# Kernel tuning notes

Hardware: AMD Instinct MI355X
Metric: run time of the kernel (lower is better)

Reference implementation:

```python
import jax, jax.numpy as jnp
import numpy as np

NUM_NODES = 1_000_000
MEM = 128
NODE_F = 172
EDGE_F = 172
EMB = 128
DECAY = 0.1
B = 16384


def setup_inputs() -> dict:
    key = jax.random.key(0)
    ks = jax.random.split(key, 32)
    g = lambda k, sh, s=0.05: (s * jax.random.normal(k, sh)).astype(jnp.float32)
    inp = {
        "src_ids": jax.random.randint(ks[0], (B,), 0, NUM_NODES),
        "dst_ids": jax.random.randint(ks[1], (B,), 0, NUM_NODES),
        "src_features": g(ks[2], (B, NODE_F), 1.0),
        "dst_features": g(ks[3], (B, NODE_F), 1.0),
        "timestamps": jax.random.uniform(ks[4], (B,), jnp.float32),
        "edge_features": g(ks[5], (B, EDGE_F), 1.0),
        # persistent state (pre-populated so decay math is non-trivial)
        "memory0": g(ks[6], (NUM_NODES, MEM), 1.0),
        "last_update0": jax.random.uniform(ks[7], (NUM_NODES,), jnp.float32),
        # edge_embedding
        "W_edge": g(ks[8], (EDGE_F, MEM)), "b_edge": jnp.zeros((MEM,), jnp.float32),
        # message_processor: Linear(MEM,MEM) -> relu -> Linear(MEM,MEM)
        "W_mp1": g(ks[9], (MEM, MEM)), "b_mp1": jnp.zeros((MEM,), jnp.float32),
        "W_mp2": g(ks[10], (MEM, MEM)), "b_mp2": jnp.zeros((MEM,), jnp.float32),
        # GRUCell(MEM, MEM), torch layout [3*MEM, MEM] (r,z,n)
        "W_ih": g(ks[11], (3 * MEM, MEM)), "W_hh": g(ks[12], (3 * MEM, MEM)),
        "b_ih": jnp.zeros((3 * MEM,), jnp.float32), "b_hh": jnp.zeros((3 * MEM,), jnp.float32),
        # node_embedding
        "W_node": g(ks[13], (NODE_F, MEM)), "b_node": jnp.zeros((MEM,), jnp.float32),
        # embedding_projection: Linear(2*MEM, EMB) -> relu -> Linear(EMB, EMB)
        "W_p1": g(ks[14], (2 * MEM, EMB)), "b_p1": jnp.zeros((EMB,), jnp.float32),
        "W_p2": g(ks[15], (EMB, EMB)), "b_p2": jnp.zeros((EMB,), jnp.float32),
        # link_predictor: Linear(2*EMB, EMB) -> relu -> Linear(EMB, 1) -> sigmoid
        "W_l1": g(ks[16], (2 * EMB, EMB)), "b_l1": jnp.zeros((EMB,), jnp.float32),
        "W_l2": g(ks[17], (EMB, 1)), "b_l2": jnp.zeros((1,), jnp.float32),
    }
    return inp


def _gru_cell(x, h, W_ih, W_hh, b_ih, b_hh):
    gi = x @ W_ih.T + b_ih
    gh = h @ W_hh.T + b_hh
    i_r, i_z, i_n = jnp.split(gi, 3, axis=-1)
    h_r, h_z, h_n = jnp.split(gh, 3, axis=-1)
    r = jax.nn.sigmoid(i_r + h_r)
    z = jax.nn.sigmoid(i_z + h_z)
    n = jnp.tanh(i_n + r * h_n)
    return (1.0 - z) * n + z * h


def reference(src_ids, dst_ids, src_features, dst_features, timestamps, edge_features,
              memory0, last_update0,
              W_edge, b_edge, W_mp1, b_mp1, W_mp2, b_mp2,
              W_ih, W_hh, b_ih, b_hh, W_node, b_node,
              W_p1, b_p1, W_p2, b_p2, W_l1, b_l1, W_l2, b_l2):
    pos = jnp.arange(B, dtype=jnp.int32)

    def update_memory(memory, last_update, ids, messages, ts):
        # batched version of the torch per-row GRU loop: current memory is
        ids = jnp.clip(ids, 0, NUM_NODES - 1)
        proc = jax.nn.relu(messages @ W_mp1 + b_mp1) @ W_mp2 + b_mp2
        dt = jnp.maximum(ts - last_update[ids], 0.0)
        cur = memory[ids] * jnp.exp(-DECAY * dt)[:, None]          # decayed get_memory
        new = _gru_cell(proc, cur, W_ih, W_hh, b_ih, b_hh)          # [B, MEM]
        last_occ = jnp.full((NUM_NODES,), -1, jnp.int32).at[ids].max(pos)
        win = last_occ[ids] == pos
        wids = jnp.where(win, ids, NUM_NODES)                       # OOB rows dropped
        memory = memory.at[wids].set(new, mode="drop")
        last_update = last_update.at[wids].set(ts, mode="drop")
        # torch does updates under no_grad into non-trainable Parameters
        return jax.lax.stop_gradient(memory), jax.lax.stop_gradient(last_update)

    def compute_embeddings(memory, last_update, ids, feats, ts):
        ids = jnp.clip(ids, 0, NUM_NODES - 1)
        dt = jnp.maximum(ts - last_update[ids], 0.0)
        score = jnp.exp(-DECAY * dt)
        mem = memory[ids] * score[:, None]       # get_memory (decayed)
        attended = mem * score[:, None]          # temporal_attention decays again (faithful)
        node_emb = feats @ W_node + b_node
        comb = jnp.concatenate([attended, node_emb], axis=1)
        emb = jax.nn.relu(comb @ W_p1 + b_p1) @ W_p2 + b_p2
        return emb, score

    edge_emb = edge_features @ W_edge + b_edge
    memory, last_update = update_memory(memory0, last_update0, src_ids, edge_emb, timestamps)
    memory, last_update = update_memory(memory, last_update, dst_ids, edge_emb, timestamps)

    src_emb, src_score = compute_embeddings(memory, last_update, src_ids, src_features, timestamps)
    dst_emb, dst_score = compute_embeddings(memory, last_update, dst_ids, dst_features, timestamps)

    link = jnp.concatenate([src_emb, dst_emb], axis=1)
    link_probs = jax.nn.sigmoid(jax.nn.relu(link @ W_l1 + b_l1) @ W_l2 + b_l2)  # [B, 1]
    return link_probs, src_score, dst_score
```

## Files before the change

### kernel.cpp

```cpp
#include <hip/hip_runtime.h>
#include <hip/hip_bf16.h>

#define B_ROWS 16384
#define NODE_F 172
#define MEMD 128
#define NN 1000000

typedef __bf16 bf16;
typedef __bf16 bf16x8 __attribute__((ext_vector_type(8)));
typedef float f32x4 __attribute__((ext_vector_type(4)));

#define W_EDGE_O 0
#define W_MP1_O  24576
#define W_MP2_O  40960
#define W_IH_O   57344
#define W_HH_O   106496
#define W_NODE_O 155648
#define W_P1_O   180224
#define W_P2_O   212992
#define W_L1_O   229376
#define W_TOTAL  262144

__device__ __forceinline__ f32x4 mfma16(bf16x8 a, bf16x8 b, f32x4 c) {
    return __builtin_amdgcn_mfma_f32_16x16x32_bf16(a, b, c, 0, 0, 0);
}

__device__ __forceinline__ int clampid(int id) {
    return id < 0 ? 0 : (id > NN - 1 ? NN - 1 : id);
}

__device__ __forceinline__ float sigmoidf_(float x) {
    return 1.f / (1.f + __expf(-x));
}

template<int NT, int KSTEPS>
__device__ __forceinline__ void gemm_wave(const bf16* Alds, int lda,
                                          const bf16* Bw, int ldb,
                                          f32x4* acc)
{
    int lane = threadIdx.x & 63;
    int p = lane & 15, q = lane >> 4;
    const bf16* ap  = Alds + p * lda + q * 8;
    const bf16* bp0 = Bw + (long)p * ldb + q * 8;
#pragma unroll
    for (int kt = 0; kt < KSTEPS; ++kt) {
        bf16x8 a = *(const bf16x8*)(ap + kt * 32);
#pragma unroll
        for (int j = 0; j < NT; ++j) {
            bf16x8 b = *(const bf16x8*)(bp0 + (long)j * 16 * ldb + kt * 32);
            acc[j] = mfma16(a, b, acc[j]);
        }
    }
}

__global__ __launch_bounds__(256) void prep_kernel(
    const float* __restrict__ W_edge, const float* __restrict__ W_mp1,
    const float* __restrict__ W_mp2, const float* __restrict__ W_ih,
    const float* __restrict__ W_hh, const float* __restrict__ W_node,
    const float* __restrict__ W_p1, const float* __restrict__ W_p2,
    const float* __restrict__ W_l1,
    int* __restrict__ last_occ, bf16* __restrict__ wb)
{
    long gid = (long)blockIdx.x * 256 + threadIdx.x;
    if (gid < NN) last_occ[gid] = -1;
    long t = gid;
    if (t < W_TOTAL) {
        float v;
        if (t < W_MP1_O)      { long u = t;            int n = u / 192, k = u % 192; v = (k < NODE_F) ? W_edge[k * 128 + n] : 0.f; }
        else if (t < W_MP2_O) { long u = t - W_MP1_O;  int n = u / 128, k = u % 128; v = W_mp1[k * 128 + n]; }
        else if (t < W_IH_O)  { long u = t - W_MP2_O;  int n = u / 128, k = u % 128; v = W_mp2[k * 128 + n]; }
        else if (t < W_HH_O)  { long u = t - W_IH_O;   v = W_ih[u]; }
        else if (t < W_NODE_O){ long u = t - W_HH_O;   v = W_hh[u]; }
        else if (t < W_P1_O)  { long u = t - W_NODE_O; int n = u / 192, k = u % 192; v = (k < NODE_F) ? W_node[k * 128 + n] : 0.f; }
        else if (t < W_P2_O)  { long u = t - W_P1_O;   int n = u / 256, k = u % 256; v = W_p1[k * 128 + n]; }
        else if (t < W_L1_O)  { long u = t - W_P2_O;   int n = u / 128, k = u % 128; v = W_p2[k * 128 + n]; }
        else                  { long u = t - W_L1_O;   int n = u / 256, k = u % 256; v = W_l1[k * 128 + n]; }
        wb[t] = (bf16)v;
    }
}

__global__ __launch_bounds__(256) void proc_kernel(
    const float* __restrict__ edgef, const bf16* __restrict__ wb,
    const float* __restrict__ b_edge, const float* __restrict__ b_mp1,
    const float* __restrict__ b_mp2, bf16* __restrict__ procB)
{
    __shared__ bf16 A0[64 * 200];
    __shared__ bf16 A1[64 * 136];
    __shared__ bf16 A2[64 * 136];
    int tid = threadIdx.x;
    long row0 = (long)blockIdx.x * 64;
    {
        int r0 = tid >> 6, c0 = tid & 63;
        for (int r = r0; r < 64; r += 4)
            for (int c = c0; c < 192; c += 64)
                A0[r * 200 + c] = (c < NODE_F) ? (bf16)edgef[(row0 + r) * NODE_F + c] : (bf16)0.f;
    }
    __syncthreads();
    int w = tid >> 6, lane = tid & 63, p = lane & 15, q = lane >> 4;
    f32x4 acc[8];
    for (int j = 0; j < 8; ++j) acc[j] = (f32x4){0.f, 0.f, 0.f, 0.f};
    gemm_wave<8, 6>(A0 + (w * 16) * 200, 200, wb + W_EDGE_O, 192, acc);
    for (int j = 0; j < 8; ++j) {
        int col = j * 16 + p;
        float bb = b_edge[col];
        for (int v = 0; v < 4; ++v)
            A1[(w * 16 + q * 4 + v) * 136 + col] = (bf16)(acc[j][v] + bb);
    }
    __syncthreads();
    for (int j = 0; j < 8; ++j) acc[j] = (f32x4){0.f, 0.f, 0.f, 0.f};
    gemm_wave<8, 4>(A1 + (w * 16) * 136, 136, wb + W_MP1_O, 128, acc);
    for (int j = 0; j < 8; ++j) {
        int col = j * 16 + p;
        float bb = b_mp1[col];
        for (int v = 0; v < 4; ++v)
            A2[(w * 16 + q * 4 + v) * 136 + col] = (bf16)fmaxf(acc[j][v] + bb, 0.f);
    }
    __syncthreads();
    for (int j = 0; j < 8; ++j) acc[j] = (f32x4){0.f, 0.f, 0.f, 0.f};
    gemm_wave<8, 4>(A2 + (w * 16) * 136, 136, wb + W_MP2_O, 128, acc);
    for (int j = 0; j < 8; ++j) {
        int col = j * 16 + p;
        float bb = b_mp2[col];
        for (int v = 0; v < 4; ++v)
            procB[(row0 + w * 16 + q * 4 + v) * 128 + col] = (bf16)(acc[j][v] + bb);
    }
}

__global__ __launch_bounds__(256) void gather_kernel(
    const int* __restrict__ ids, const float* __restrict__ ts,
    const float* __restrict__ memory, const float* __restrict__ last_update,
    int* __restrict__ last_occ, float* __restrict__ cur, int tagbase)
{
    __shared__ float sc_s[32];
    __shared__ int id_s[32];
    int tid = threadIdx.x;
    int rb = blockIdx.x * 32;
    if (tid < 32) {
        int rid = rb + tid;
        int id = clampid(ids[rid]);
        float dtv = fmaxf(ts[rid] - last_update[id], 0.f);
        float sc = __expf(-0.1f * dtv);
        sc_s[tid] = sc; id_s[tid] = id;
        atomicMax(&last_occ[id], tagbase + rid);
    }
    __syncthreads();
    const f32x4* mem4 = (const f32x4*)memory;
    f32x4* cur4 = (f32x4*)cur;
    for (int idx = tid; idx < 32 * 32; idx += 256) {
        int r = idx >> 5, c4 = idx & 31;
        f32x4 v = mem4[(long)id_s[r] * 32 + c4];
        float s = sc_s[r];
        v.x *= s; v.y *= s; v.z *= s; v.w *= s;
        cur4[(long)(rb + r) * 32 + c4] = v;
    }
}

__global__ __launch_bounds__(256) void gru_kernel(
    const int* __restrict__ ids, const float* __restrict__ ts,
    const bf16* __restrict__ procB, const float* __restrict__ cur,
    const bf16* __restrict__ wb, const float* __restrict__ b_ih,
    const float* __restrict__ b_hh, const int* __restrict__ last_occ,
    float* __restrict__ memory, float* __restrict__ last_update, int tagbase)
{
    __shared__ bf16 Ap[16 * 136];
    __shared__ bf16 Ac[16 * 136];
    __shared__ float sA[16 * 384];
    __shared__ float sB[16 * 384];
    __shared__ int id_s[16];
    __shared__ int win_s[16];
    int tid = threadIdx.x;
    int rb = blockIdx.x * 16;
    if (tid < 16) {
        int rid = rb + tid;
        int id = clampid(ids[rid]);
        id_s[tid] = id;
        int win = (last_occ[id] == tagbase + rid) ? 1 : 0;
        win_s[tid] = win;
        if (win) last_update[id] = ts[rid];
    }
    {
        int r = tid >> 4, c8 = tid & 15;
        *(bf16x8*)&Ap[r * 136 + c8 * 8] = *(const bf16x8*)&procB[(long)(rb + r) * 128 + c8 * 8];
        f32x4 v0 = *(const f32x4*)&cur[(long)(rb + r) * 128 + c8 * 8];
        f32x4 v1 = *(const f32x4*)&cur[(long)(rb + r) * 128 + c8 * 8 + 4];
        bf16x8 cb;
        cb[0] = (bf16)v0.x; cb[1] = (bf16)v0.y; cb[2] = (bf16)v0.z; cb[3] = (bf16)v0.w;
        cb[4] = (bf16)v1.x; cb[5] = (bf16)v1.y; cb[6] = (bf16)v1.z; cb[7] = (bf16)v1.w;
        *(bf16x8*)&Ac[r * 136 + c8 * 8] = cb;
    }
    __syncthreads();
    int w = tid >> 6, lane = tid & 63, p = lane & 15, q = lane >> 4;
#pragma unroll
    for (int j = 0; j < 12; ++j) {
        int cidx = w * 12 + j;
        bool is_gi = cidx < 24;
        int nt = is_gi ? cidx : cidx - 24;
        const bf16* Al = (is_gi ? Ap : Ac) + p * 136 + q * 8;
        const bf16* Bw = wb + (is_gi ? W_IH_O : W_HH_O) + (long)(nt * 16 + p) * 128 + q * 8;
        f32x4 acc = (f32x4){0.f, 0.f, 0.f, 0.f};
#pragma unroll
        for (int kt = 0; kt < 4; ++kt) {
            bf16x8 a = *(const bf16x8*)(Al + kt * 32);
            bf16x8 b = *(const bf16x8*)(Bw + kt * 32);
            acc = mfma16(a, b, acc);
        }
        float* S = is_gi ? sA : sB;
        int col = nt * 16 + p;
        for (int v = 0; v < 4; ++v) S[(q * 4 + v) * 384 + col] = acc[v];
    }
    __syncthreads();
    for (int idx = tid; idx < 16 * 128; idx += 256) {
        int r = idx >> 7, c = idx & 127;
        float ir = sA[r * 384 + c]       + b_ih[c];
        float iz = sA[r * 384 + 128 + c] + b_ih[128 + c];
        float in_ = sA[r * 384 + 256 + c] + b_ih[256 + c];
        float hr = sB[r * 384 + c]       + b_hh[c];
        float hz = sB[r * 384 + 128 + c] + b_hh[128 + c];
        float hn = sB[r * 384 + 256 + c] + b_hh[256 + c];
        float rg = sigmoidf_(ir + hr);
        float zg = sigmoidf_(iz + hz);
        float ng = tanhf(in_ + rg * hn);
        float h = cur[(long)(rb + r) * 128 + c];
        float nv = (1.f - zg) * ng + zg * h;
        if (win_s[r]) memory[(long)id_s[r] * 128 + c] = nv;
    }
}

__global__ __launch_bounds__(256) void emb_kernel(
    const int* __restrict__ src_ids, const int* __restrict__ dst_ids,
    const float* __restrict__ src_feat, const float* __restrict__ dst_feat,
    const float* __restrict__ ts, const float* __restrict__ memory,
    const float* __restrict__ last_update, const bf16* __restrict__ wb,
    const float* __restrict__ b_node, const float* __restrict__ b_p1,
    const float* __restrict__ b_p2, bf16* __restrict__ embS,
    bf16* __restrict__ embD, float* __restrict__ dout)
{
    int side = blockIdx.y;
    const int* ids = side ? dst_ids : src_ids;
    const float* feats = side ? dst_feat : src_feat;
    bf16* embOut = side ? embD : embS;
    __shared__ bf16 A0[64 * 200];
    __shared__ bf16 Comb[64 * 264];
    __shared__ bf16 A2[64 * 136];
    __shared__ float sc_s[64];
    __shared__ int id_s[64];
    int tid = threadIdx.x;
    long row0 = (long)blockIdx.x * 64;
    if (tid < 64) {
        int rid = (int)row0 + tid;
        int id = clampid(ids[rid]);
        float dtv = fmaxf(ts[rid] - last_update[id], 0.f);
        float sc = __expf(-0.1f * dtv);
        sc_s[tid] = sc; id_s[tid] = id;
        dout[B_ROWS + side * B_ROWS + rid] = sc;
    }
    {
        int r0 = tid >> 6, c0 = tid & 63;
        for (int r = r0; r < 64; r += 4)
            for (int c = c0; c < 192; c += 64)
                A0[r * 200 + c] = (c < NODE_F) ? (bf16)feats[(row0 + r) * NODE_F + c] : (bf16)0.f;
    }
    __syncthreads();
    {
        const f32x4* mem4 = (const f32x4*)memory;
        for (int idx = tid; idx < 64 * 32; idx += 256) {
            int r = idx >> 5, c4 = idx & 31;
            float s = sc_s[r]; s = s * s;
            f32x4 v = mem4[(long)id_s[r] * 32 + c4];
            int base = r * 264 + c4 * 4;
            Comb[base + 0] = (bf16)(v.x * s);
            Comb[base + 1] = (bf16)(v.y * s);
            Comb[base + 2] = (bf16)(v.z * s);
            Comb[base + 3] = (bf16)(v.w * s);
        }
    }
    __syncthreads();
    int w = tid >> 6, lane = tid & 63, p = lane & 15, q = lane >> 4;
    f32x4 acc[8];
    for (int j = 0; j < 8; ++j) acc[j] = (f32x4){0.f, 0.f, 0.f, 0.f};
    gemm_wave<8, 6>(A0 + (w * 16) * 200, 200, wb + W_NODE_O, 192, acc);
    for (int j = 0; j < 8; ++j) {
        int col = j * 16 + p;
        float bb = b_node[col];
        for (int v = 0; v < 4; ++v)
            Comb[(w * 16 + q * 4 + v) * 264 + 128 + col] = (bf16)(acc[j][v] + bb);
    }
    __syncthreads();
    for (int j = 0; j < 8; ++j) acc[j] = (f32x4){0.f, 0.f, 0.f, 0.f};
    gemm_wave<8, 8>(Comb + (w * 16) * 264, 264, wb + W_P1_O, 256, acc);
    for (int j = 0; j < 8; ++j) {
        int col = j * 16 + p;
        float bb = b_p1[col];
        for (int v = 0; v < 4; ++v)
            A2[(w * 16 + q * 4 + v) * 136 + col] = (bf16)fmaxf(acc[j][v] + bb, 0.f);
    }
    __syncthreads();
    for (int j = 0; j < 8; ++j) acc[j] = (f32x4){0.f, 0.f, 0.f, 0.f};
    gemm_wave<8, 4>(A2 + (w * 16) * 136, 136, wb + W_P2_O, 128, acc);
    for (int j = 0; j < 8; ++j) {
        int col = j * 16 + p;
        float bb = b_p2[col];
        for (int v = 0; v < 4; ++v)
            embOut[(row0 + w * 16 + q * 4 + v) * 128 + col] = (bf16)(acc[j][v] + bb);
    }
}

__global__ __launch_bounds__(256) void link_kernel(
    const bf16* __restrict__ embS, const bf16* __restrict__ embD,
    const bf16* __restrict__ wb, const float* __restrict__ b_l1,
    const float* __restrict__ W_l2, const float* __restrict__ b_l2,
    float* __restrict__ out)
{
    __shared__ bf16 A[64 * 264];
    __shared__ float H[64 * 132];
    int tid = threadIdx.x;
    long row0 = (long)blockIdx.x * 64;
    for (int g = tid; g < 64 * 32; g += 256) {
        int r = g >> 5, c8 = g & 31;
        const bf16* src = (c8 < 16) ? &embS[(row0 + r) * 128 + c8 * 8]
                                    : &embD[(row0 + r) * 128 + (c8 - 16) * 8];
        *(bf16x8*)&A[r * 264 + c8 * 8] = *(const bf16x8*)src;
    }
    __syncthreads();
    int w = tid >> 6, lane = tid & 63, p = lane & 15, q = lane >> 4;
    f32x4 acc[8];
    for (int j = 0; j < 8; ++j) acc[j] = (f32x4){0.f, 0.f, 0.f, 0.f};
    gemm_wave<8, 8>(A + (w * 16) * 264, 264, wb + W_L1_O, 256, acc);
    for (int j = 0; j < 8; ++j) {
        int col = j * 16 + p;
        float bb = b_l1[col];
        for (int v = 0; v < 4; ++v)
            H[(w * 16 + q * 4 + v) * 132 + col] = fmaxf(acc[j][v] + bb, 0.f);
    }
    __syncthreads();
    if (tid < 64) {
        float a = b_l2[0];
        for (int c = 0; c < 128; ++c) a += H[tid * 132 + c] * W_l2[c];
        out[row0 + tid] = sigmoidf_(a);
    }
}

extern "C" void kernel_launch(void* const* d_in, const int* in_sizes, int n_in,
                              void* d_out, int out_size, void* d_ws, size_t ws_size,
                              hipStream_t stream)
{
    const int*   src_ids  = (const int*)d_in[0];
    const int*   dst_ids  = (const int*)d_in[1];
    const float* src_feat = (const float*)d_in[2];
    const float* dst_feat = (const float*)d_in[3];
    const float* ts       = (const float*)d_in[4];
    const float* edgef    = (const float*)d_in[5];
    float* memory         = (float*)d_in[6];
    float* last_update    = (float*)d_in[7];
    const float* W_edge = (const float*)d_in[8],  *b_edge = (const float*)d_in[9];
    const float* W_mp1  = (const float*)d_in[10], *b_mp1  = (const float*)d_in[11];
    const float* W_mp2  = (const float*)d_in[12], *b_mp2  = (const float*)d_in[13];
    const float* W_ih   = (const float*)d_in[14], *W_hh   = (const float*)d_in[15];
    const float* b_ih   = (const float*)d_in[16], *b_hh   = (const float*)d_in[17];
    const float* W_node = (const float*)d_in[18], *b_node = (const float*)d_in[19];
    const float* W_p1   = (const float*)d_in[20], *b_p1   = (const float*)d_in[21];
    const float* W_p2   = (const float*)d_in[22], *b_p2   = (const float*)d_in[23];
    const float* W_l1   = (const float*)d_in[24], *b_l1   = (const float*)d_in[25];
    const float* W_l2   = (const float*)d_in[26], *b_l2   = (const float*)d_in[27];

    char* ws = (char*)d_ws;
    int*   last_occ = (int*)ws;
    bf16*  wb       = (bf16*)(ws + 4000000);
    bf16*  procB    = (bf16*)(ws + 4524288);
    float* cur      = (float*)(ws + 8718592);
    bf16*  embS     = (bf16*)(ws + 17107200);
    bf16*  embD     = (bf16*)(ws + 21301504);
    float* dout     = (float*)d_out;

    prep_kernel<<<3907, 256, 0, stream>>>(W_edge, W_mp1, W_mp2, W_ih, W_hh,
                                          W_node, W_p1, W_p2, W_l1, last_occ, wb);
    proc_kernel<<<256, 256, 0, stream>>>(edgef, wb, b_edge, b_mp1, b_mp2, procB);
    gather_kernel<<<512, 256, 0, stream>>>(src_ids, ts, memory, last_update,
                                           last_occ, cur, 0);
    gru_kernel<<<1024, 256, 0, stream>>>(src_ids, ts, procB, cur, wb, b_ih, b_hh,
                                         last_occ, memory, last_update, 0);
    gather_kernel<<<512, 256, 0, stream>>>(dst_ids, ts, memory, last_update,
                                           last_occ, cur, B_ROWS);
    gru_kernel<<<1024, 256, 0, stream>>>(dst_ids, ts, procB, cur, wb, b_ih, b_hh,
                                         last_occ, memory, last_update, B_ROWS);
    emb_kernel<<<dim3(256, 2), 256, 0, stream>>>(src_ids, dst_ids, src_feat, dst_feat,
                                                 ts, memory, last_update, wb,
                                                 b_node, b_p1, b_p2, embS, embD, dout);
    link_kernel<<<256, 256, 0, stream>>>(embS, embD, wb, b_l1, W_l2, b_l2, dout);
}
```

Before: 800.2 us.

## Stop writing the persistent memory table; keep per-row GRU outputs and redirect reads

After: 779.9 us. 1.03x faster.

```diff
diff --git a/kernel.cpp b/kernel.cpp
--- a/kernel.cpp
+++ b/kernel.cpp
@@ -31,6 +31,10 @@
 
 __device__ __forceinline__ float sigmoidf_(float x) {
     return 1.f / (1.f + __expf(-x));
+}
+
+__device__ __forceinline__ float tanhf_(float x) {
+    return 1.f - 2.f / (__expf(2.f * x) + 1.f);
 }
 
 template<int NT, int KSTEPS>
@@ -59,22 +63,26 @@
     const float* __restrict__ W_hh, const float* __restrict__ W_node,
     const float* __restrict__ W_p1, const float* __restrict__ W_p2,
     const float* __restrict__ W_l1,
-    int* __restrict__ last_occ, bf16* __restrict__ wb)
-{
-    long gid = (long)blockIdx.x * 256 + threadIdx.x;
-    if (gid < NN) last_occ[gid] = -1;
-    long t = gid;
+    int* __restrict__ occS, int* __restrict__ occD, bf16* __restrict__ wb)
+{
+    int gid = blockIdx.x * 256 + threadIdx.x;
+    if (gid < NN / 4) {
+        int4 m1 = {-1, -1, -1, -1};
+        ((int4*)occS)[gid] = m1;
+        ((int4*)occD)[gid] = m1;
+    }
+    int t = gid;
     if (t < W_TOTAL) {
         float v;
-        if (t < W_MP1_O)      { long u = t;            int n = u / 192, k = u % 192; v = (k < NODE_F) ? W_edge[k * 128 + n] : 0.f; }
-        else if (t < W_MP2_O) { long u = t - W_MP1_O;  int n = u / 128, k = u % 128; v = W_mp1[k * 128 + n]; }
-        else if (t < W_IH_O)  { long u = t - W_MP2_O;  int n = u / 128, k = u % 128; v = W_mp2[k * 128 + n]; }
-        else if (t < W_HH_O)  { long u = t - W_IH_O;   v = W_ih[u]; }
-        else if (t < W_NODE_O){ long u = t - W_HH_O;   v = W_hh[u]; }
-        else if (t < W_P1_O)  { long u = t - W_NODE_O; int n = u / 192, k = u % 192; v = (k < NODE_F) ? W_node[k * 128 + n] : 0.f; }
-        else if (t < W_P2_O)  { long u = t - W_P1_O;   int n = u / 256, k = u % 256; v = W_p1[k * 128 + n]; }
-        else if (t < W_L1_O)  { long u = t - W_P2_O;   int n = u / 128, k = u % 128; v = W_p2[k * 128 + n]; }
-        else                  { long u = t - W_L1_O;   int n = u / 256, k = u % 256; v = W_l1[k * 128 + n]; }
+        if (t < W_MP1_O)      { int u = t;            int n = u / 192, k = u % 192; v = (k < NODE_F) ? W_edge[k * 128 + n] : 0.f; }
+        else if (t < W_MP2_O) { int u = t - W_MP1_O;  int n = u / 128, k = u % 128; v = W_mp1[k * 128 + n]; }
+        else if (t < W_IH_O)  { int u = t - W_MP2_O;  int n = u / 128, k = u % 128; v = W_mp2[k * 128 + n]; }
+        else if (t < W_HH_O)  { int u = t - W_IH_O;   v = W_ih[u]; }
+        else if (t < W_NODE_O){ int u = t - W_HH_O;   v = W_hh[u]; }
+        else if (t < W_P1_O)  { int u = t - W_NODE_O; int n = u / 192, k = u % 192; v = (k < NODE_F) ? W_node[k * 128 + n] : 0.f; }
+        else if (t < W_P2_O)  { int u = t - W_P1_O;   int n = u / 256, k = u % 256; v = W_p1[k * 128 + n]; }
+        else if (t < W_L1_O)  { int u = t - W_P2_O;   int n = u / 128, k = u % 128; v = W_p2[k * 128 + n]; }
+        else                  { int u = t - W_L1_O;   int n = u / 256, k = u % 256; v = W_l1[k * 128 + n]; }
         wb[t] = (bf16)v;
     }
 }
@@ -82,13 +90,20 @@
 __global__ __launch_bounds__(256) void proc_kernel(
     const float* __restrict__ edgef, const bf16* __restrict__ wb,
     const float* __restrict__ b_edge, const float* __restrict__ b_mp1,
-    const float* __restrict__ b_mp2, bf16* __restrict__ procB)
+    const float* __restrict__ b_mp2, const int* __restrict__ src_ids,
+    const int* __restrict__ dst_ids, int* __restrict__ occS,
+    int* __restrict__ occD, bf16* __restrict__ procB)
 {
     __shared__ bf16 A0[64 * 200];
     __shared__ bf16 A1[64 * 136];
     __shared__ bf16 A2[64 * 136];
     int tid = threadIdx.x;
     long row0 = (long)blockIdx.x * 64;
+    if (tid < 64) {
+        int rid = (int)row0 + tid;
+        atomicMax(&occS[clampid(src_ids[rid])], rid);
+        atomicMax(&occD[clampid(dst_ids[rid])], rid);
+    }
     {
         int r0 = tid >> 6, c0 = tid & 63;
         for (int r = r0; r < 64; r += 4)
@@ -126,63 +141,47 @@
     }
 }
 
-__global__ __launch_bounds__(256) void gather_kernel(
-    const int* __restrict__ ids, const float* __restrict__ ts,
-    const float* __restrict__ memory, const float* __restrict__ last_update,
-    int* __restrict__ last_occ, float* __restrict__ cur, int tagbase)
-{
-    __shared__ float sc_s[32];
-    __shared__ int id_s[32];
-    int tid = threadIdx.x;
-    int rb = blockIdx.x * 32;
-    if (tid < 32) {
-        int rid = rb + tid;
-        int id = clampid(ids[rid]);
-        float dtv = fmaxf(ts[rid] - last_update[id], 0.f);
-        float sc = __expf(-0.1f * dtv);
-        sc_s[tid] = sc; id_s[tid] = id;
-        atomicMax(&last_occ[id], tagbase + rid);
-    }
-    __syncthreads();
-    const f32x4* mem4 = (const f32x4*)memory;
-    f32x4* cur4 = (f32x4*)cur;
-    for (int idx = tid; idx < 32 * 32; idx += 256) {
-        int r = idx >> 5, c4 = idx & 31;
-        f32x4 v = mem4[(long)id_s[r] * 32 + c4];
-        float s = sc_s[r];
-        v.x *= s; v.y *= s; v.z *= s; v.w *= s;
-        cur4[(long)(rb + r) * 32 + c4] = v;
-    }
-}
-
 __global__ __launch_bounds__(256) void gru_kernel(
     const int* __restrict__ ids, const float* __restrict__ ts,
-    const bf16* __restrict__ procB, const float* __restrict__ cur,
-    const bf16* __restrict__ wb, const float* __restrict__ b_ih,
-    const float* __restrict__ b_hh, const int* __restrict__ last_occ,
-    float* __restrict__ memory, float* __restrict__ last_update, int tagbase)
+    const bf16* __restrict__ procB, const float* __restrict__ memory,
+    const float* __restrict__ last_update, const int* __restrict__ occPrev,
+    const float* __restrict__ newmemPrev, const bf16* __restrict__ wb,
+    const float* __restrict__ b_ih, const float* __restrict__ b_hh,
+    float* __restrict__ newmemOut, int round)
 {
     __shared__ bf16 Ap[16 * 136];
     __shared__ bf16 Ac[16 * 136];
+    __shared__ float curF[16 * 128];
     __shared__ float sA[16 * 384];
     __shared__ float sB[16 * 384];
-    __shared__ int id_s[16];
-    __shared__ int win_s[16];
+    __shared__ float sc_s[16];
+    __shared__ const float* rowp_s[16];
     int tid = threadIdx.x;
     int rb = blockIdx.x * 16;
     if (tid < 16) {
         int rid = rb + tid;
         int id = clampid(ids[rid]);
-        id_s[tid] = id;
-        int win = (last_occ[id] == tagbase + rid) ? 1 : 0;
-        win_s[tid] = win;
-        if (win) last_update[id] = ts[rid];
-    }
+        const float* rowp = &memory[(long)id * MEMD];
+        float lu = last_update[id];
+        if (round) {
+            int tg = occPrev[id];
+            if (tg >= 0) { rowp = &newmemPrev[(long)tg * MEMD]; lu = ts[tg]; }
+        }
+        float dtv = fmaxf(ts[rid] - lu, 0.f);
+        sc_s[tid] = __expf(-0.1f * dtv);
+        rowp_s[tid] = rowp;
+    }
+    __syncthreads();
     {
         int r = tid >> 4, c8 = tid & 15;
         *(bf16x8*)&Ap[r * 136 + c8 * 8] = *(const bf16x8*)&procB[(long)(rb + r) * 128 + c8 * 8];
-        f32x4 v0 = *(const f32x4*)&cur[(long)(rb + r) * 128 + c8 * 8];
-        f32x4 v1 = *(const f32x4*)&cur[(long)(rb + r) * 128 + c8 * 8 + 4];
+        float s = sc_s[r];
+        f32x4 v0 = *(const f32x4*)(rowp_s[r] + c8 * 8);
+        f32x4 v1 = *(const f32x4*)(rowp_s[r] + c8 * 8 + 4);
+        v0.x *= s; v0.y *= s; v0.z *= s; v0.w *= s;
+        v1.x *= s; v1.y *= s; v1.z *= s; v1.w *= s;
+        *(f32x4*)&curF[r * 128 + c8 * 8] = v0;
+        *(f32x4*)&curF[r * 128 + c8 * 8 + 4] = v1;
         bf16x8 cb;
         cb[0] = (bf16)v0.x; cb[1] = (bf16)v0.y; cb[2] = (bf16)v0.z; cb[3] = (bf16)v0.w;
         cb[4] = (bf16)v1.x; cb[5] = (bf16)v1.y; cb[6] = (bf16)v1.z; cb[7] = (bf16)v1.w;
@@ -211,18 +210,17 @@
     __syncthreads();
     for (int idx = tid; idx < 16 * 128; idx += 256) {
         int r = idx >> 7, c = idx & 127;
-        float ir = sA[r * 384 + c]       + b_ih[c];
-        float iz = sA[r * 384 + 128 + c] + b_ih[128 + c];
+        float ir = sA[r * 384 + c]        + b_ih[c];
+        float iz = sA[r * 384 + 128 + c]  + b_ih[128 + c];
         float in_ = sA[r * 384 + 256 + c] + b_ih[256 + c];
-        float hr = sB[r * 384 + c]       + b_hh[c];
-        float hz = sB[r * 384 + 128 + c] + b_hh[128 + c];
-        float hn = sB[r * 384 + 256 + c] + b_hh[256 + c];
+        float hr = sB[r * 384 + c]        + b_hh[c];
+        float hz = sB[r * 384 + 128 + c]  + b_hh[128 + c];
+        float hn = sB[r * 384 + 256 + c]  + b_hh[256 + c];
         float rg = sigmoidf_(ir + hr);
         float zg = sigmoidf_(iz + hz);
-        float ng = tanhf(in_ + rg * hn);
-        float h = cur[(long)(rb + r) * 128 + c];
-        float nv = (1.f - zg) * ng + zg * h;
-        if (win_s[r]) memory[(long)id_s[r] * 128 + c] = nv;
+        float ng = tanhf_(in_ + rg * hn);
+        float h = curF[r * 128 + c];
+        newmemOut[(long)(rb + r) * 128 + c] = (1.f - zg) * ng + zg * h;
     }
 }
 
@@ -230,7 +228,9 @@
     const int* __restrict__ src_ids, const int* __restrict__ dst_ids,
     const float* __restrict__ src_feat, const float* __restrict__ dst_feat,
     const float* __restrict__ ts, const float* __restrict__ memory,
-    const float* __restrict__ last_update, const bf16* __restrict__ wb,
+    const float* __restrict__ last_update, const int* __restrict__ occS,
+    const int* __restrict__ occD, const float* __restrict__ newmemS,
+    const float* __restrict__ newmemD, const bf16* __restrict__ wb,
     const float* __restrict__ b_node, const float* __restrict__ b_p1,
     const float* __restrict__ b_p2, bf16* __restrict__ embS,
     bf16* __restrict__ embD, float* __restrict__ dout)
@@ -243,15 +243,20 @@
     __shared__ bf16 Comb[64 * 264];
     __shared__ bf16 A2[64 * 136];
     __shared__ float sc_s[64];
-    __shared__ int id_s[64];
+    __shared__ const float* rowp_s[64];
     int tid = threadIdx.x;
     long row0 = (long)blockIdx.x * 64;
     if (tid < 64) {
         int rid = (int)row0 + tid;
         int id = clampid(ids[rid]);
-        float dtv = fmaxf(ts[rid] - last_update[id], 0.f);
+        const float* rowp = &memory[(long)id * MEMD];
+        float lu = last_update[id];
+        int tgD = occD[id], tgS = occS[id];
+        if (tgD >= 0)      { rowp = &newmemD[(long)tgD * MEMD]; lu = ts[tgD]; }
+        else if (tgS >= 0) { rowp = &newmemS[(long)tgS * MEMD]; lu = ts[tgS]; }
+        float dtv = fmaxf(ts[rid] - lu, 0.f);
         float sc = __expf(-0.1f * dtv);
-        sc_s[tid] = sc; id_s[tid] = id;
+        sc_s[tid] = sc; rowp_s[tid] = rowp;
         dout[B_ROWS + side * B_ROWS + rid] = sc;
     }
     {
@@ -262,16 +267,17 @@
     }
     __syncthreads();
     {
-        const f32x4* mem4 = (const f32x4*)memory;
-        for (int idx = tid; idx < 64 * 32; idx += 256) {
-            int r = idx >> 5, c4 = idx & 31;
+        for (int idx = tid; idx < 64 * 16; idx += 256) {
+            int r = idx >> 4, c8 = idx & 15;
             float s = sc_s[r]; s = s * s;
-            f32x4 v = mem4[(long)id_s[r] * 32 + c4];
-            int base = r * 264 + c4 * 4;
-            Comb[base + 0] = (bf16)(v.x * s);
-            Comb[base + 1] = (bf16)(v.y * s);
-            Comb[base + 2] = (bf16)(v.z * s);
-            Comb[base + 3] = (bf16)(v.w * s);
+            f32x4 v0 = *(const f32x4*)(rowp_s[r] + c8 * 8);
+            f32x4 v1 = *(const f32x4*)(rowp_s[r] + c8 * 8 + 4);
+            bf16x8 cb;
+            cb[0] = (bf16)(v0.x * s); cb[1] = (bf16)(v0.y * s);
+            cb[2] = (bf16)(v0.z * s); cb[3] = (bf16)(v0.w * s);
+            cb[4] = (bf16)(v1.x * s); cb[5] = (bf16)(v1.y * s);
+            cb[6] = (bf16)(v1.z * s); cb[7] = (bf16)(v1.w * s);
+            *(bf16x8*)&Comb[r * 264 + c8 * 8] = cb;
         }
     }
     __syncthreads();
@@ -350,8 +356,8 @@
     const float* dst_feat = (const float*)d_in[3];
     const float* ts       = (const float*)d_in[4];
     const float* edgef    = (const float*)d_in[5];
-    float* memory         = (float*)d_in[6];
-    float* last_update    = (float*)d_in[7];
+    const float* memory   = (const float*)d_in[6];
+    const float* last_update = (const float*)d_in[7];
     const float* W_edge = (const float*)d_in[8],  *b_edge = (const float*)d_in[9];
     const float* W_mp1  = (const float*)d_in[10], *b_mp1  = (const float*)d_in[11];
     const float* W_mp2  = (const float*)d_in[12], *b_mp2  = (const float*)d_in[13];
@@ -364,27 +370,27 @@
     const float* W_l2   = (const float*)d_in[26], *b_l2   = (const float*)d_in[27];
 
     char* ws = (char*)d_ws;
-    int*   last_occ = (int*)ws;
-    bf16*  wb       = (bf16*)(ws + 4000000);
-    bf16*  procB    = (bf16*)(ws + 4524288);
-    float* cur      = (float*)(ws + 8718592);
-    bf16*  embS     = (bf16*)(ws + 17107200);
-    bf16*  embD     = (bf16*)(ws + 21301504);
+    int*   occS     = (int*)ws;
+    int*   occD     = (int*)(ws + 4000000);
+    bf16*  wb       = (bf16*)(ws + 8000000);
+    bf16*  procB    = (bf16*)(ws + 8524288);
+    float* newmemS  = (float*)(ws + 12718592);
+    float* newmemD  = (float*)(ws + 21107200);
+    bf16*  embS     = (bf16*)(ws + 29495808);
+    bf16*  embD     = (bf16*)(ws + 33690112);
     float* dout     = (float*)d_out;
 
-    prep_kernel<<<3907, 256, 0, stream>>>(W_edge, W_mp1, W_mp2, W_ih, W_hh,
-                                          W_node, W_p1, W_p2, W_l1, last_occ, wb);
-    proc_kernel<<<256, 256, 0, stream>>>(edgef, wb, b_edge, b_mp1, b_mp2, procB);
-    gather_kernel<<<512, 256, 0, stream>>>(src_ids, ts, memory, last_update,
-                                           last_occ, cur, 0);
-    gru_kernel<<<1024, 256, 0, stream>>>(src_ids, ts, procB, cur, wb, b_ih, b_hh,
-                                         last_occ, memory, last_update, 0);
-    gather_kernel<<<512, 256, 0, stream>>>(dst_ids, ts, memory, last_update,
-                                           last_occ, cur, B_ROWS);
-    gru_kernel<<<1024, 256, 0, stream>>>(dst_ids, ts, procB, cur, wb, b_ih, b_hh,
-                                         last_occ, memory, last_update, B_ROWS);
+    prep_kernel<<<1024, 256, 0, stream>>>(W_edge, W_mp1, W_mp2, W_ih, W_hh,
+                                          W_node, W_p1, W_p2, W_l1, occS, occD, wb);
+    proc_kernel<<<256, 256, 0, stream>>>(edgef, wb, b_edge, b_mp1, b_mp2,
+                                         src_ids, dst_ids, occS, occD, procB);
+    gru_kernel<<<1024, 256, 0, stream>>>(src_ids, ts, procB, memory, last_update,
+                                         occS, newmemS, wb, b_ih, b_hh, newmemS, 0);
+    gru_kernel<<<1024, 256, 0, stream>>>(dst_ids, ts, procB, memory, last_update,
+                                         occS, newmemS, wb, b_ih, b_hh, newmemD, 1);
     emb_kernel<<<dim3(256, 2), 256, 0, stream>>>(src_ids, dst_ids, src_feat, dst_feat,
-                                                 ts, memory, last_update, wb,
+                                                 ts, memory, last_update, occS, occD,
+                                                 newmemS, newmemD, wb,
                                                  b_node, b_p1, b_p2, embS, embD, dout);
     link_kernel<<<256, 256, 0, stream>>>(embS, embD, wb, b_l1, W_l2, b_l2, dout);
 }
```
